# Optimization experiments

Measured on AMD Instinct MI355X. Metric: run time of the kernel, lower is better.

The kernel has to match this reference:

```python
import jax, jax.numpy as jnp
import numpy as np

EMBED_DIM = 256
NUM_HEADS = 8


def positional_encoding(max_seq_len, embed_dim):
    # Faithful to torch source: exponent uses 2*i/embed_dim with raw column index i;
    # row 0 is all zeros; sin on even cols, cos on odd cols for rows 1:.
    pos = jnp.arange(max_seq_len, dtype=jnp.float32)[:, None]          # [L,1]
    i = jnp.arange(embed_dim, dtype=jnp.float32)[None, :]              # [1,D]
    angles = pos / jnp.power(10000.0, 2.0 * i / embed_dim)             # [L,D]
    pe = jnp.where((jnp.arange(embed_dim) % 2 == 0)[None, :],
                   jnp.sin(angles), jnp.cos(angles))
    pe = pe.at[0].set(0.0)
    return pe


def setup_inputs() -> dict:
    key = jax.random.key(0)
    ks = jax.random.split(key, 9)
    b, c, h, w = 4, EMBED_DIM, 48, 48
    d = EMBED_DIM  # internal_dim (downsample_rate=1)
    s = 1.0 / np.sqrt(d)
    inp = {
        "x": jax.random.normal(ks[0], (b, c, h, w), dtype=jnp.float32),
        "wq": jax.random.uniform(ks[1], (d, d), jnp.float32, -s, s),
        "bq": jax.random.uniform(ks[2], (d,), jnp.float32, -s, s),
        "wk": jax.random.uniform(ks[3], (d, d), jnp.float32, -s, s),
        "bk": jax.random.uniform(ks[4], (d,), jnp.float32, -s, s),
        "wv": jax.random.uniform(ks[5], (d, d), jnp.float32, -s, s),
        "bv": jax.random.uniform(ks[6], (d,), jnp.float32, -s, s),
        "wo": jax.random.uniform(ks[7], (d, d), jnp.float32, -s, s),
        "bo": jax.random.uniform(ks[8], (d,), jnp.float32, -s, s),
    }
    return inp


def reference(x, wq, bq, wk, bk, wv, bv, wo, bo):
    b, c, h, w = x.shape
    n = h * w
    H = NUM_HEADS
    dh = c // H
    xs = x.reshape(b, c, n).transpose(0, 2, 1)            # [b, n, c]
    xs = xs + positional_encoding(n, c)[None]             # add PE
    q = xs @ wq.T + bq                                    # [b, n, c]
    k = xs @ wk.T + bk
    v = xs @ wv.T + bv
    # separate heads -> [b, H, n, dh]
    q = q.reshape(b, n, H, dh).transpose(0, 2, 1, 3)
    k = k.reshape(b, n, H, dh).transpose(0, 2, 1, 3)
    v = v.reshape(b, n, H, dh).transpose(0, 2, 1, 3)
    attn = jnp.einsum("bhqd,bhkd->bhqk", q, k) / jnp.sqrt(jnp.float32(dh))
    attn = jax.nn.softmax(attn, axis=-1)
    out = jnp.einsum("bhqk,bhkd->bhqd", attn, v)          # [b, H, n, dh]
    out = out.transpose(0, 2, 1, 3).reshape(b, n, c)      # recombine heads
    out = out @ wo.T + bo                                 # out_proj
    return out.transpose(0, 2, 1).reshape(b, c, h, w)
```

## Files before the change

### kernel.cpp

```cpp
#include <hip/hip_runtime.h>

#define EMBED 256
#define NPOS  2304
#define BATCH 4
#define NH    8
#define DH    32

typedef float f32x4  __attribute__((ext_vector_type(4)));
typedef short bf16x8 __attribute__((ext_vector_type(8)));
typedef short s16x4  __attribute__((ext_vector_type(4)));
typedef unsigned u32x4 __attribute__((ext_vector_type(4)));

static __device__ __forceinline__ short f2b(float f) {
    union { float f; unsigned u; } c; c.f = f;
    unsigned r = (c.u + 0x7FFFu + ((c.u >> 16) & 1u)) >> 16;
    return (short)r;
}

static __device__ __forceinline__ unsigned cvtpk(float lo, float hi) {
    unsigned r;
    asm("v_cvt_pk_bf16_f32 %0, %1, %2" : "=v"(r) : "v"(lo), "v"(hi));
    return r;
}

static __device__ __forceinline__ float fexp2(float x) {
    float r;
    asm("v_exp_f32 %0, %1" : "=v"(r) : "v"(x));
    return r;
}

static __device__ __forceinline__ void plswap32(unsigned& a, unsigned& b) {
    asm("v_permlane32_swap_b32 %0, %1" : "+v"(a), "+v"(b));
}
static __device__ __forceinline__ void plswap16(unsigned& a, unsigned& b) {
    asm("v_permlane16_swap_b32 %0, %1" : "+v"(a), "+v"(b));
}

static __device__ __forceinline__ void gl_lds16(const short* g, short* l) {
    __builtin_amdgcn_global_load_lds(
        (const __attribute__((address_space(1))) unsigned int*)(g),
        (__attribute__((address_space(3))) unsigned int*)(l),
        16, 0, 0);
}

__global__ __launch_bounds__(256) void prep_all(
        const float* __restrict__ x,
        const float* __restrict__ wq, const float* __restrict__ wk,
        const float* __restrict__ wv, const float* __restrict__ wo,
        short* __restrict__ wqkv, short* __restrict__ wob,
        short* __restrict__ xs) {
    __shared__ float xt[32][65];
    int blk = blockIdx.x;
    int t = threadIdx.x;
    if (blk < 1024) {
        int g = blk * 256 + t;
        if (g < 196608) {
            int j = g >> 8, kk = g & 255;
            int proj = j >> 8, jj = j & 255;
            const float* s = (proj == 0) ? wq : (proj == 1) ? wk : wv;
            wqkv[g] = f2b(s[jj * 256 + kk]);
        } else if (g < 262144) {
            int h2 = g - 196608;
            wob[h2] = f2b(wo[h2]);
        }
        return;
    }
    int bx = blk - 1024;
    int b = bx / 288, rem = bx % 288;
    int c0 = (rem / 36) * 32, pos0 = (rem % 36) * 64;
    int j = t & 63, i0 = t >> 6;
    const float* xp = x + (size_t)(b * EMBED + c0) * NPOS + pos0;
#pragma unroll
    for (int rr = 0; rr < 8; ++rr) {
        int i = rr * 4 + i0;
        xt[i][j] = xp[(size_t)i * NPOS + j];
    }
    __syncthreads();
    int ii = (t & 15) * 2, jj0 = t >> 4;
    const float kln = -0.07195578415606394f;
#pragma unroll
    for (int pp = 0; pp < 4; ++pp) {
        int jj = pp * 16 + jj0;
        int pos = pos0 + jj;
        float v0 = xt[ii][jj], v1 = xt[ii + 1][jj];
        float pe0 = 0.f, pe1 = 0.f;
        if (pos > 0) {
            int c = c0 + ii;
            float a0 = (float)pos * __expf((float)c * kln);
            float a1 = (float)pos * __expf((float)(c + 1) * kln);
            pe0 = __sinf(a0);
            pe1 = __cosf(a1);
        }
        unsigned lo = (unsigned short)f2b(v0 + pe0);
        unsigned hi = (unsigned short)f2b(v1 + pe1);
        *reinterpret_cast<unsigned*>(xs + (size_t)(b * NPOS + pos) * EMBED + c0 + ii) =
            lo | (hi << 16);
    }
}

__global__ __launch_bounds__(256) void gemm_qkv(
        const short* __restrict__ A, const short* __restrict__ Bw,
        const float* __restrict__ bq, const float* __restrict__ bk,
        const float* __restrict__ bv,
        short* __restrict__ qd, short* __restrict__ kd, short* __restrict__ vtd) {
    __shared__ short a_sm[64 * 64];
    __shared__ short b_sm[64 * 64];
    int bx = blockIdx.x;
    int bm = bx / 12, bn = bx % 12;
    int m0 = bm * 64, n0 = bn * 64;
    int t = threadIdx.x;
    int lane = t & 63, wid = t >> 6;
    int wm = wid >> 1, wn = wid & 1;
    int l15 = lane & 15, l4 = lane >> 4;

    f32x4 acc[2][2];
#pragma unroll
    for (int ni = 0; ni < 2; ++ni) {
        int jcol = n0 + wn * 32 + ni * 16 + l15;
        int proj = jcol >> 8, jj = jcol & 255;
        float bias = ((proj == 0) ? bq : (proj == 1) ? bk : bv)[jj];
        f32x4 bi = {bias, bias, bias, bias};
        acc[0][ni] = bi;
        acc[1][ni] = bi;
    }

    int srow = t >> 2, sblk = t & 3;
    const short* ag = &A[(size_t)(m0 + srow) * 256 + sblk * 8];
    const short* bg = &Bw[(size_t)(n0 + srow) * 256 + sblk * 8];
    int sw0 = ((sblk ^ (srow & 7)) * 8);
    int sw1 = (((sblk + 4) ^ (srow & 7)) * 8);
    short* al0 = &a_sm[srow * 64 + sw0];
    short* al1 = &a_sm[srow * 64 + sw1];
    short* bl0 = &b_sm[srow * 64 + sw0];
    short* bl1 = &b_sm[srow * 64 + sw1];

    for (int ks = 0; ks < 4; ++ks) {
        __syncthreads();
        *(bf16x8*)al0 = *(const bf16x8*)(ag + ks * 64);
        *(bf16x8*)al1 = *(const bf16x8*)(ag + ks * 64 + 32);
        *(bf16x8*)bl0 = *(const bf16x8*)(bg + ks * 64);
        *(bf16x8*)bl1 = *(const bf16x8*)(bg + ks * 64 + 32);
        __syncthreads();
#pragma unroll
        for (int kk = 0; kk < 2; ++kk) {
            bf16x8 af[2], bf[2];
#pragma unroll
            for (int mi = 0; mi < 2; ++mi) {
                int ar = wm * 32 + mi * 16 + l15;
                int blk = kk * 4 + l4;
                af[mi] = *(const bf16x8*)&a_sm[ar * 64 + ((blk ^ (ar & 7)) * 8)];
            }
#pragma unroll
            for (int ni = 0; ni < 2; ++ni) {
                int br = wn * 32 + ni * 16 + l15;
                int blk = kk * 4 + l4;
                bf[ni] = *(const bf16x8*)&b_sm[br * 64 + ((blk ^ (br & 7)) * 8)];
            }
#pragma unroll
            for (int mi = 0; mi < 2; ++mi)
#pragma unroll
                for (int ni = 0; ni < 2; ++ni)
                    acc[mi][ni] = __builtin_amdgcn_mfma_f32_16x16x32_bf16(
                        af[mi], bf[ni], acc[mi][ni], 0, 0, 0);
        }
    }

    const float qs = 0.2550348623f;
#pragma unroll
    for (int mi = 0; mi < 2; ++mi) {
        int rowb = m0 + wm * 32 + mi * 16 + l4 * 4;
        int b = rowb / NPOS;
        int pos = rowb - b * NPOS;
#pragma unroll
        for (int ni = 0; ni < 2; ++ni) {
            int jcol = n0 + wn * 32 + ni * 16 + l15;
            int proj = jcol >> 8, jj = jcol & 255;
            int h = jj >> 5, d = jj & 31;
            if (proj == 2) {
                s16x4 pk;
#pragma unroll
                for (int r = 0; r < 4; ++r) pk[r] = f2b(acc[mi][ni][r]);
                *(s16x4*)&vtd[((size_t)(b * NH + h) * DH + d) * NPOS + pos] = pk;
            } else {
                short* dst = (proj == 0) ? qd : kd;
                float sc = (proj == 0) ? qs : 1.0f;
#pragma unroll
                for (int r = 0; r < 4; ++r)
                    dst[((size_t)(b * NH + h) * NPOS + pos + r) * DH + d] =
                        f2b(acc[mi][ni][r] * sc);
            }
        }
    }
}


__global__ __launch_bounds__(256) void attn_fwd(
        const short* __restrict__ Q, const short* __restrict__ K,
        const short* __restrict__ VT, short* __restrict__ AO) {
    __shared__ short smem[16384];

    int bx0 = blockIdx.x;
    int bx = (bx0 & 7) * 144 + (bx0 >> 3);
    int bh = bx / 36, qg = bx % 36;
    int q0 = qg * 64;
    int t = threadIdx.x, lane = t & 63, wid = t >> 6;
    int l15 = lane & 15, l4 = lane >> 4;

    const short* Qb = Q + ((size_t)bh * NPOS + q0) * DH;
    bf16x8 qf[4];
#pragma unroll
    for (int qt = 0; qt < 4; ++qt)
        qf[qt] = *(const bf16x8*)&Qb[(qt * 16 + l15) * DH + l4 * 8];

    int kv0 = wid * 576;
    int ra = lane >> 2, blk = lane & 3;
    int swzk = (ra >> 1) & 3;
    int swzv = (ra & 3) ^ ((ra >> 2) & 3);
    const short* kga = K + ((size_t)bh * NPOS + kv0 + ra) * DH + ((blk ^ swzk) * 8);
    const short* vga = VT + ((size_t)bh * DH + ra) * NPOS + kv0 + ((blk ^ swzv) * 8);

    short* kbuf = smem + wid * 4096;
    short* vbuf = kbuf + 2048;

#pragma unroll
    for (int p = 0; p < 2; ++p) {
        gl_lds16(kga + p * 1024,            kbuf + p * 1024);
        gl_lds16(kga + p * 1024 + 16 * DH,  kbuf + p * 1024 + 512);
        gl_lds16(vga + p * 32,              vbuf + p * 1024);
        gl_lds16(vga + p * 32 + 16 * NPOS,  vbuf + p * 1024 + 512);
    }

    f32x4 zero = {0.f, 0.f, 0.f, 0.f};
    f32x4 o[2][4];
    f32x4 lacc[4];
#pragma unroll
    for (int qt = 0; qt < 4; ++qt) { o[0][qt] = zero; o[1][qt] = zero; lacc[qt] = zero; }
    const float MB = -17.312340490667561f;
    const f32x4 mb = {MB, MB, MB, MB};
    const u32x4 ones_u = {0x3F803F80u, 0x3F803F80u, 0x3F803F80u, 0x3F803F80u};
    const bf16x8 ones = __builtin_bit_cast(bf16x8, ones_u);

    int kswr = (l4 ^ ((l15 >> 1) & 3)) * 8;
    int vswr = (l4 ^ ((l15 & 3) ^ ((l15 >> 2) & 3))) * 8;

#pragma unroll 1
    for (int tt = 0; tt < 18; ++tt) {
        int buf = tt & 1;
        if (tt < 17) asm volatile("s_waitcnt vmcnt(4)" ::: "memory");
        else         asm volatile("s_waitcnt vmcnt(0)" ::: "memory");

        const short* kb = kbuf + buf * 1024;
        const short* vb = vbuf + buf * 1024;
        bf16x8 kf0 = *(const bf16x8*)&kb[l15 * 32 + kswr];
        bf16x8 kf1 = *(const bf16x8*)&kb[(16 + l15) * 32 + kswr];
        bf16x8 vf0 = *(const bf16x8*)&vb[l15 * 32 + vswr];
        bf16x8 vf1 = *(const bf16x8*)&vb[(16 + l15) * 32 + vswr];
        asm volatile("s_waitcnt lgkmcnt(0)" ::: "memory");
        __builtin_amdgcn_sched_barrier(0);

        if (tt + 2 < 18) {
            gl_lds16(kga + (tt + 2) * 1024,            kbuf + buf * 1024);
            gl_lds16(kga + (tt + 2) * 1024 + 16 * DH,  kbuf + buf * 1024 + 512);
            gl_lds16(vga + (tt + 2) * 32,              vbuf + buf * 1024);
            gl_lds16(vga + (tt + 2) * 32 + 16 * NPOS,  vbuf + buf * 1024 + 512);
        }

        __builtin_amdgcn_s_setprio(1);
#pragma unroll
        for (int qt = 0; qt < 4; ++qt) {
            f32x4 s0 = __builtin_amdgcn_mfma_f32_16x16x32_bf16(kf0, qf[qt], mb, 0, 0, 0);
            f32x4 s1 = __builtin_amdgcn_mfma_f32_16x16x32_bf16(kf1, qf[qt], mb, 0, 0, 0);

            float e00 = fexp2(s0[0]), e01 = fexp2(s0[1]), e02 = fexp2(s0[2]), e03 = fexp2(s0[3]);
            float e10 = fexp2(s1[0]), e11 = fexp2(s1[1]), e12 = fexp2(s1[2]), e13 = fexp2(s1[3]);

            unsigned p00 = cvtpk(e00, e01), p01 = cvtpk(e02, e03);
            unsigned p10 = cvtpk(e10, e11), p11 = cvtpk(e12, e13);
            unsigned a0 = p00, b0 = p10;
            plswap32(a0, b0); plswap16(a0, b0);
            unsigned a1 = p01, b1 = p11;
            plswap32(a1, b1); plswap16(a1, b1);
            u32x4 fr = {a0, a1, b0, b1};
            bf16x8 pf = __builtin_bit_cast(bf16x8, fr);

            o[0][qt] = __builtin_amdgcn_mfma_f32_16x16x32_bf16(vf0, pf, o[0][qt], 0, 0, 0);
            o[1][qt] = __builtin_amdgcn_mfma_f32_16x16x32_bf16(vf1, pf, o[1][qt], 0, 0, 0);
            lacc[qt] = __builtin_amdgcn_mfma_f32_16x16x32_bf16(ones, pf, lacc[qt], 0, 0, 0);
        }
        __builtin_amdgcn_s_setprio(0);
    }


    __syncthreads();
    if (wid > 0) {
        f32x4* od = (f32x4*)(smem + wid * 4096);
#pragma unroll
        for (int qt = 0; qt < 4; ++qt) {
#pragma unroll
            for (int dt = 0; dt < 2; ++dt)
                od[(qt * 2 + dt) * 64 + lane] = o[dt][qt];
        }
        if (l4 == 0) {
            float* ld = (float*)smem;
#pragma unroll
            for (int qt = 0; qt < 4; ++qt)
                ld[(wid - 1) * 64 + qt * 16 + l15] = lacc[qt][0];
        }
    }
    __syncthreads();
    if (wid == 0) {
        int b = bh >> 3, h = bh & 7;
        const float* ld = (const float*)smem;
#pragma unroll
        for (int qt = 0; qt < 4; ++qt) {
            float lt = lacc[qt][0] + ld[qt * 16 + l15] + ld[64 + qt * 16 + l15]
                     + ld[128 + qt * 16 + l15];
            float inv = __builtin_amdgcn_rcpf(lt);
            int qrow = q0 + qt * 16 + l15;
            size_t obase = ((size_t)b * NPOS + qrow) * EMBED + h * DH;
#pragma unroll
            for (int dt = 0; dt < 2; ++dt) {
                f32x4 ot = o[dt][qt];
#pragma unroll
                for (int w = 1; w < 4; ++w)
                    ot += ((const f32x4*)(smem + w * 4096))[(qt * 2 + dt) * 64 + lane];
                unsigned x0 = cvtpk(ot[0] * inv, ot[1] * inv);
                unsigned x1 = cvtpk(ot[2] * inv, ot[3] * inv);
                *(unsigned long long*)&AO[obase + dt * 16 + l4 * 4] =
                    (unsigned long long)x0 | ((unsigned long long)x1 << 32);
            }
        }
    }
}

__global__ __launch_bounds__(256) void gemm_out(
        const short* __restrict__ A, const short* __restrict__ Bw,
        const float* __restrict__ bo, float* __restrict__ out) {
    __shared__ short a_sm[32 * 64];
    __shared__ short b_sm[64 * 64];
    int bx = blockIdx.x;
    int bm = bx >> 2, bn = bx & 3;
    int m0 = bm * 32, n0 = bn * 64;
    int t = threadIdx.x;
    int lane = t & 63, wid = t >> 6;
    int wm = wid >> 1, wn = wid & 1;
    int l15 = lane & 15, l4 = lane >> 4;

    f32x4 acc[2];
#pragma unroll
    for (int ni = 0; ni < 2; ++ni) {
        float bias = bo[n0 + wn * 32 + ni * 16 + l15];
        f32x4 bi = {bias, bias, bias, bias};
        acc[ni] = bi;
    }

    int srow = t >> 2, sblk = t & 3;
    const short* ag = &A[(size_t)(m0 + srow) * 256 + sblk * 8];
    const short* bg = &Bw[(size_t)(n0 + srow) * 256 + sblk * 8];
    int sw0 = ((sblk ^ (srow & 7)) * 8);
    int sw1 = (((sblk + 4) ^ (srow & 7)) * 8);
    short* al0 = &a_sm[srow * 64 + sw0];
    short* al1 = &a_sm[srow * 64 + sw1];
    short* bl0 = &b_sm[srow * 64 + sw0];
    short* bl1 = &b_sm[srow * 64 + sw1];

    for (int ks = 0; ks < 4; ++ks) {
        __syncthreads();
        if (t < 128) {
            *(bf16x8*)al0 = *(const bf16x8*)(ag + ks * 64);
            *(bf16x8*)al1 = *(const bf16x8*)(ag + ks * 64 + 32);
        }
        *(bf16x8*)bl0 = *(const bf16x8*)(bg + ks * 64);
        *(bf16x8*)bl1 = *(const bf16x8*)(bg + ks * 64 + 32);
        __syncthreads();
#pragma unroll
        for (int kk = 0; kk < 2; ++kk) {
            int blk = kk * 4 + l4;
            int ar = wm * 16 + l15;
            bf16x8 af = *(const bf16x8*)&a_sm[ar * 64 + ((blk ^ (ar & 7)) * 8)];
            bf16x8 bf[2];
#pragma unroll
            for (int ni = 0; ni < 2; ++ni) {
                int br = wn * 32 + ni * 16 + l15;
                bf[ni] = *(const bf16x8*)&b_sm[br * 64 + ((blk ^ (br & 7)) * 8)];
            }
#pragma unroll
            for (int ni = 0; ni < 2; ++ni)
                acc[ni] = __builtin_amdgcn_mfma_f32_16x16x32_bf16(af, bf[ni], acc[ni], 0, 0, 0);
        }
    }

    int rowb = m0 + wm * 16 + l4 * 4;
    int b = rowb / NPOS;
    int pos = rowb - b * NPOS;
#pragma unroll
    for (int ni = 0; ni < 2; ++ni) {
        int jcol = n0 + wn * 32 + ni * 16 + l15;
        *(f32x4*)&out[((size_t)(b * EMBED) + jcol) * NPOS + pos] = acc[ni];
    }
}

extern "C" void kernel_launch(void* const* d_in, const int* in_sizes, int n_in,
                              void* d_out, int out_size, void* d_ws, size_t ws_size,
                              hipStream_t stream) {
    const float* x  = (const float*)d_in[0];
    const float* wq = (const float*)d_in[1];
    const float* bq = (const float*)d_in[2];
    const float* wk = (const float*)d_in[3];
    const float* bk = (const float*)d_in[4];
    const float* wv = (const float*)d_in[5];
    const float* bv = (const float*)d_in[6];
    const float* wo = (const float*)d_in[7];
    const float* bo = (const float*)d_in[8];

    char* ws = (char*)d_ws;
    short* wqkv = (short*)(ws);
    short* wob  = (short*)(ws + 393216);
    short* xs   = (short*)(ws + 524288);
    short* qb   = (short*)(ws + 5242880);
    short* kb   = (short*)(ws + 9961472);
    short* vtb  = (short*)(ws + 14680064);
    short* ao   = (short*)(ws + 19398656);
    float* out  = (float*)d_out;

    hipLaunchKernelGGL(prep_all, dim3(2176), dim3(256), 0, stream,
                       x, wq, wk, wv, wo, wqkv, wob, xs);
    hipLaunchKernelGGL(gemm_qkv, dim3(1728), dim3(256), 0, stream,
                       xs, wqkv, bq, bk, bv, qb, kb, vtb);
    hipLaunchKernelGGL(attn_fwd, dim3(1152), dim3(256), 0, stream, qb, kb, vtb, ao);
    hipLaunchKernelGGL(gemm_out, dim3(1152), dim3(256), 0, stream, ao, wob, bo, out);
}
```

Baseline: 71.43 us.

## Split attention waves into KV-pair groups sharing K/V tiles across query halves

```diff
diff --git a/kernel.cpp b/kernel.cpp
--- a/kernel.cpp
+++ b/kernel.cpp
@@ -197,44 +197,48 @@
 __global__ __launch_bounds__(256) void attn_fwd(
         const short* __restrict__ Q, const short* __restrict__ K,
         const short* __restrict__ VT, short* __restrict__ AO) {
-    __shared__ short smem[16384];
+    __shared__ short smem[8192];
 
     int bx0 = blockIdx.x;
     int bx = (bx0 & 7) * 144 + (bx0 >> 3);
     int bh = bx / 36, qg = bx % 36;
     int q0 = qg * 64;
     int t = threadIdx.x, lane = t & 63, wid = t >> 6;
+    int pr = wid >> 1, rg = wid & 1;
     int l15 = lane & 15, l4 = lane >> 4;
 
-    const short* Qb = Q + ((size_t)bh * NPOS + q0) * DH;
-    bf16x8 qf[4];
-#pragma unroll
-    for (int qt = 0; qt < 4; ++qt)
-        qf[qt] = *(const bf16x8*)&Qb[(qt * 16 + l15) * DH + l4 * 8];
-
-    int kv0 = wid * 576;
+    const short* Qb = Q + ((size_t)bh * NPOS + q0 + rg * 32) * DH;
+    bf16x8 qf[2];
+    qf[0] = *(const bf16x8*)&Qb[l15 * DH + l4 * 8];
+    qf[1] = *(const bf16x8*)&Qb[(16 + l15) * DH + l4 * 8];
+
+    int kv0 = pr * 1152;
     int ra = lane >> 2, blk = lane & 3;
     int swzk = (ra >> 1) & 3;
     int swzv = (ra & 3) ^ ((ra >> 2) & 3);
     const short* kga = K + ((size_t)bh * NPOS + kv0 + ra) * DH + ((blk ^ swzk) * 8);
     const short* vga = VT + ((size_t)bh * DH + ra) * NPOS + kv0 + ((blk ^ swzv) * 8);
 
-    short* kbuf = smem + wid * 4096;
+    short* kbuf = smem + pr * 4096;
     short* vbuf = kbuf + 2048;
 
-#pragma unroll
-    for (int p = 0; p < 2; ++p) {
-        gl_lds16(kga + p * 1024,            kbuf + p * 1024);
-        gl_lds16(kga + p * 1024 + 16 * DH,  kbuf + p * 1024 + 512);
-        gl_lds16(vga + p * 32,              vbuf + p * 1024);
-        gl_lds16(vga + p * 32 + 16 * NPOS,  vbuf + p * 1024 + 512);
+    if (rg == 0) {
+        gl_lds16(kga,                   kbuf);
+        gl_lds16(kga + 16 * DH,         kbuf + 512);
+        gl_lds16(kga + 1024,            kbuf + 1024);
+        gl_lds16(kga + 1024 + 16 * DH,  kbuf + 1536);
+    } else {
+        gl_lds16(vga,                   vbuf);
+        gl_lds16(vga + 16 * NPOS,       vbuf + 512);
+        gl_lds16(vga + 32,              vbuf + 1024);
+        gl_lds16(vga + 32 + 16 * NPOS,  vbuf + 1536);
     }
 
     f32x4 zero = {0.f, 0.f, 0.f, 0.f};
-    f32x4 o[2][4];
-    f32x4 lacc[4];
-#pragma unroll
-    for (int qt = 0; qt < 4; ++qt) { o[0][qt] = zero; o[1][qt] = zero; lacc[qt] = zero; }
+    f32x4 o[2][2];
+    f32x4 lacc[2];
+    o[0][0] = zero; o[0][1] = zero; o[1][0] = zero; o[1][1] = zero;
+    lacc[0] = zero; lacc[1] = zero;
     const float MB = -17.312340490667561f;
     const f32x4 mb = {MB, MB, MB, MB};
     const u32x4 ones_u = {0x3F803F80u, 0x3F803F80u, 0x3F803F80u, 0x3F803F80u};
@@ -244,10 +248,11 @@
     int vswr = (l4 ^ ((l15 & 3) ^ ((l15 >> 2) & 3))) * 8;
 
 #pragma unroll 1
-    for (int tt = 0; tt < 18; ++tt) {
+    for (int tt = 0; tt < 36; ++tt) {
         int buf = tt & 1;
-        if (tt < 17) asm volatile("s_waitcnt vmcnt(4)" ::: "memory");
+        if (tt < 35) asm volatile("s_waitcnt vmcnt(2)" ::: "memory");
         else         asm volatile("s_waitcnt vmcnt(0)" ::: "memory");
+        __builtin_amdgcn_s_barrier();
 
         const short* kb = kbuf + buf * 1024;
         const short* vb = vbuf + buf * 1024;
@@ -257,17 +262,20 @@
         bf16x8 vf1 = *(const bf16x8*)&vb[(16 + l15) * 32 + vswr];
         asm volatile("s_waitcnt lgkmcnt(0)" ::: "memory");
         __builtin_amdgcn_sched_barrier(0);
-
-        if (tt + 2 < 18) {
-            gl_lds16(kga + (tt + 2) * 1024,            kbuf + buf * 1024);
-            gl_lds16(kga + (tt + 2) * 1024 + 16 * DH,  kbuf + buf * 1024 + 512);
-            gl_lds16(vga + (tt + 2) * 32,              vbuf + buf * 1024);
-            gl_lds16(vga + (tt + 2) * 32 + 16 * NPOS,  vbuf + buf * 1024 + 512);
-        }
-
-        __builtin_amdgcn_s_setprio(1);
-#pragma unroll
-        for (int qt = 0; qt < 4; ++qt) {
+        __builtin_amdgcn_s_barrier();
+
+        if (tt + 2 < 36) {
+            if (rg == 0) {
+                gl_lds16(kga + (tt + 2) * 1024,           kbuf + buf * 1024);
+                gl_lds16(kga + (tt + 2) * 1024 + 16 * DH, kbuf + buf * 1024 + 512);
+            } else {
+                gl_lds16(vga + (tt + 2) * 32,             vbuf + buf * 1024);
+                gl_lds16(vga + (tt + 2) * 32 + 16 * NPOS, vbuf + buf * 1024 + 512);
+            }
+        }
+
+#pragma unroll
+        for (int qt = 0; qt < 2; ++qt) {
             f32x4 s0 = __builtin_amdgcn_mfma_f32_16x16x32_bf16(kf0, qf[qt], mb, 0, 0, 0);
             f32x4 s1 = __builtin_amdgcn_mfma_f32_16x16x32_bf16(kf1, qf[qt], mb, 0, 0, 0);
 
@@ -287,43 +295,38 @@
             o[1][qt] = __builtin_amdgcn_mfma_f32_16x16x32_bf16(vf1, pf, o[1][qt], 0, 0, 0);
             lacc[qt] = __builtin_amdgcn_mfma_f32_16x16x32_bf16(ones, pf, lacc[qt], 0, 0, 0);
         }
-        __builtin_amdgcn_s_setprio(0);
     }
 
 
     __syncthreads();
-    if (wid > 0) {
-        f32x4* od = (f32x4*)(smem + wid * 4096);
-#pragma unroll
-        for (int qt = 0; qt < 4; ++qt) {
+    if (pr == 1) {
+        f32x4* od = (f32x4*)(smem + 4096) + rg * 256;
+#pragma unroll
+        for (int qt = 0; qt < 2; ++qt)
 #pragma unroll
             for (int dt = 0; dt < 2; ++dt)
                 od[(qt * 2 + dt) * 64 + lane] = o[dt][qt];
-        }
         if (l4 == 0) {
             float* ld = (float*)smem;
 #pragma unroll
-            for (int qt = 0; qt < 4; ++qt)
-                ld[(wid - 1) * 64 + qt * 16 + l15] = lacc[qt][0];
+            for (int qt = 0; qt < 2; ++qt)
+                ld[rg * 32 + qt * 16 + l15] = lacc[qt][0];
         }
     }
     __syncthreads();
-    if (wid == 0) {
+    if (pr == 0) {
+        const float* ld = (const float*)smem;
+        const f32x4* od = (const f32x4*)(smem + 4096) + rg * 256;
         int b = bh >> 3, h = bh & 7;
-        const float* ld = (const float*)smem;
-#pragma unroll
-        for (int qt = 0; qt < 4; ++qt) {
-            float lt = lacc[qt][0] + ld[qt * 16 + l15] + ld[64 + qt * 16 + l15]
-                     + ld[128 + qt * 16 + l15];
+#pragma unroll
+        for (int qt = 0; qt < 2; ++qt) {
+            float lt = lacc[qt][0] + ld[rg * 32 + qt * 16 + l15];
             float inv = __builtin_amdgcn_rcpf(lt);
-            int qrow = q0 + qt * 16 + l15;
+            int qrow = q0 + rg * 32 + qt * 16 + l15;
             size_t obase = ((size_t)b * NPOS + qrow) * EMBED + h * DH;
 #pragma unroll
             for (int dt = 0; dt < 2; ++dt) {
-                f32x4 ot = o[dt][qt];
-#pragma unroll
-                for (int w = 1; w < 4; ++w)
-                    ot += ((const f32x4*)(smem + w * 4096))[(qt * 2 + dt) * 64 + lane];
+                f32x4 ot = o[dt][qt] + od[(qt * 2 + dt) * 64 + lane];
                 unsigned x0 = cvtpk(ot[0] * inv, ot[1] * inv);
                 unsigned x1 = cvtpk(ot[2] * inv, ot[3] * inv);
                 *(unsigned long long*)&AO[obase + dt * 16 + l4 * 4] =
```

New measurement: 72.28 us. About the same (+1.2%).

## Tile V-transpose into contiguous 32x32 blocks and vectorize weight conversion

Applied to the files above, without the earlier changes.

```diff
diff --git a/kernel.cpp b/kernel.cpp
--- a/kernel.cpp
+++ b/kernel.cpp
@@ -52,20 +52,28 @@
     __shared__ float xt[32][65];
     int blk = blockIdx.x;
     int t = threadIdx.x;
-    if (blk < 1024) {
-        int g = blk * 256 + t;
-        if (g < 196608) {
-            int j = g >> 8, kk = g & 255;
+    if (blk < 256) {
+        int g4 = (blk * 256 + t) * 4;
+        if (g4 < 196608) {
+            int j = g4 >> 8, kk = g4 & 255;
             int proj = j >> 8, jj = j & 255;
             const float* s = (proj == 0) ? wq : (proj == 1) ? wk : wv;
-            wqkv[g] = f2b(s[jj * 256 + kk]);
-        } else if (g < 262144) {
-            int h2 = g - 196608;
-            wob[h2] = f2b(wo[h2]);
+            f32x4 w = *(const f32x4*)&s[jj * 256 + kk];
+            s16x4 o4;
+#pragma unroll
+            for (int r = 0; r < 4; ++r) o4[r] = f2b(w[r]);
+            *(s16x4*)&wqkv[g4] = o4;
+        } else {
+            int h2 = g4 - 196608;
+            f32x4 w = *(const f32x4*)&wo[h2];
+            s16x4 o4;
+#pragma unroll
+            for (int r = 0; r < 4; ++r) o4[r] = f2b(w[r]);
+            *(s16x4*)&wob[h2] = o4;
         }
         return;
     }
-    int bx = blk - 1024;
+    int bx = blk - 256;
     int b = bx / 288, rem = bx % 288;
     int c0 = (rem / 36) * 32, pos0 = (rem % 36) * 64;
     int j = t & 63, i0 = t >> 6;
@@ -180,7 +188,8 @@
                 s16x4 pk;
 #pragma unroll
                 for (int r = 0; r < 4; ++r) pk[r] = f2b(acc[mi][ni][r]);
-                *(s16x4*)&vtd[((size_t)(b * NH + h) * DH + d) * NPOS + pos] = pk;
+                *(s16x4*)&vtd[(((size_t)(b * NH + h) * 72 + (pos >> 5)) << 10)
+                              + d * 32 + (pos & 31)] = pk;
             } else {
                 short* dst = (proj == 0) ? qd : kd;
                 float sc = (proj == 0) ? qs : 1.0f;
@@ -217,7 +226,8 @@
     int swzk = (ra >> 1) & 3;
     int swzv = (ra & 3) ^ ((ra >> 2) & 3);
     const short* kga = K + ((size_t)bh * NPOS + kv0 + ra) * DH + ((blk ^ swzk) * 8);
-    const short* vga = VT + ((size_t)bh * DH + ra) * NPOS + kv0 + ((blk ^ swzv) * 8);
+    const short* vga = VT + (((size_t)bh * 72 + wid * 18) << 10)
+                          + ra * 32 + ((blk ^ swzv) * 8);
 
     short* kbuf = smem + wid * 4096;
     short* vbuf = kbuf + 2048;
@@ -226,8 +236,8 @@
     for (int p = 0; p < 2; ++p) {
         gl_lds16(kga + p * 1024,            kbuf + p * 1024);
         gl_lds16(kga + p * 1024 + 16 * DH,  kbuf + p * 1024 + 512);
-        gl_lds16(vga + p * 32,              vbuf + p * 1024);
-        gl_lds16(vga + p * 32 + 16 * NPOS,  vbuf + p * 1024 + 512);
+        gl_lds16(vga + p * 1024,            vbuf + p * 1024);
+        gl_lds16(vga + p * 1024 + 512,      vbuf + p * 1024 + 512);
     }
 
     f32x4 zero = {0.f, 0.f, 0.f, 0.f};
@@ -261,8 +271,8 @@
         if (tt + 2 < 18) {
             gl_lds16(kga + (tt + 2) * 1024,            kbuf + buf * 1024);
             gl_lds16(kga + (tt + 2) * 1024 + 16 * DH,  kbuf + buf * 1024 + 512);
-            gl_lds16(vga + (tt + 2) * 32,              vbuf + buf * 1024);
-            gl_lds16(vga + (tt + 2) * 32 + 16 * NPOS,  vbuf + buf * 1024 + 512);
+            gl_lds16(vga + (tt + 2) * 1024,            vbuf + buf * 1024);
+            gl_lds16(vga + (tt + 2) * 1024 + 512,      vbuf + buf * 1024 + 512);
         }
 
         __builtin_amdgcn_s_setprio(1);
@@ -423,7 +433,7 @@
     short* ao   = (short*)(ws + 19398656);
     float* out  = (float*)d_out;
 
-    hipLaunchKernelGGL(prep_all, dim3(2176), dim3(256), 0, stream,
+    hipLaunchKernelGGL(prep_all, dim3(1408), dim3(256), 0, stream,
                        x, wq, wk, wv, wo, wqkv, wob, xs);
     hipLaunchKernelGGL(gemm_qkv, dim3(1728), dim3(256), 0, stream,
                        xs, wqkv, bq, bk, bv, qb, kb, vtb);
```

After: 70.70 us. About the same (-1.0%).
